# Kernel optimization log

Hardware: AMD Instinct MI355X
Metric: run time of the kernel (lower is better)

Reference implementation:

```python
import jax, jax.numpy as jnp
import numpy as np

N, E, H, L, IN_DIM, OUT_DIM = 50000, 500000, 128, 6, 3, 9


def _lin_init(k, fi, fo):
    W = jax.random.normal(k, (fi, fo), jnp.float32) / np.sqrt(fi)
    return W, jnp.zeros((fo,), jnp.float32)


def setup_inputs() -> dict:
    key = jax.random.key(0)
    ks = jax.random.split(key, 40)
    inp = {}
    inp['x'] = jax.random.normal(ks[0], (N, IN_DIM), jnp.float32)
    inp['coords'] = jax.random.uniform(ks[1], (N, 3), jnp.float32)
    inp['edge_index'] = jax.random.randint(ks[2], (2, E), 0, N, jnp.int64)
    # encoders
    inp['W_ne1'], inp['b_ne1'] = _lin_init(ks[3], IN_DIM, H)
    inp['W_ne2'], inp['b_ne2'] = _lin_init(ks[4], H, H)
    inp['W_ee1'], inp['b_ee1'] = _lin_init(ks[5], 4, H)
    inp['W_ee2'], inp['b_ee2'] = _lin_init(ks[6], H, H)
    # per-layer params, stacked over L
    def stack(fn):
        Ws, bs = zip(*[fn(l) for l in range(L)])
        return jnp.stack(Ws), jnp.stack(bs)
    inp['We1'], inp['be1'] = stack(lambda l: _lin_init(ks[7 + l], 3 * H, H))
    inp['We2'], inp['be2'] = stack(lambda l: _lin_init(ks[13 + l], H, H))
    inp['Wn1'], inp['bn1'] = stack(lambda l: _lin_init(ks[19 + l], 2 * H, H))
    inp['Wn2'], inp['bn2'] = stack(lambda l: _lin_init(ks[25 + l], H, H))
    inp['ln_g'] = jnp.ones((L, H), jnp.float32)
    inp['ln_b'] = jnp.zeros((L, H), jnp.float32)
    # decoder
    inp['Wd1'], inp['bd1'] = _lin_init(ks[31], H, H)
    inp['Wd2'], inp['bd2'] = _lin_init(ks[32], H, OUT_DIM)
    return inp


def _mlp2(x, W1, b1, W2, b2):
    return jax.nn.silu(x @ W1 + b1) @ W2 + b2


def _layernorm(x, g, b, eps=1e-5):
    m = jnp.mean(x, -1, keepdims=True)
    v = jnp.mean(jnp.square(x - m), -1, keepdims=True)
    return (x - m) / jnp.sqrt(v + eps) * g + b


def reference(x, coords, edge_index,
              W_ne1, b_ne1, W_ne2, b_ne2, W_ee1, b_ee1, W_ee2, b_ee2,
              We1, be1, We2, be2, Wn1, bn1, Wn2, bn2, ln_g, ln_b,
              Wd1, bd1, Wd2, bd2):
    src, dst = edge_index[0], edge_index[1]
    # edge features: relative displacement + distance -> (E,4)
    rel = coords[dst] - coords[src]
    ef = jnp.concatenate([rel, jnp.linalg.norm(rel, axis=-1, keepdims=True)], -1)
    edge_attr = _mlp2(ef, W_ee1, b_ee1, W_ee2, b_ee2)  # (E,H)
    h = _mlp2(x, W_ne1, b_ne1, W_ne2, b_ne2)           # (N,H)
    # in-degree for mean aggregation (PyG mean -> 0 for isolated nodes)
    deg = jax.ops.segment_sum(jnp.ones((E,), h.dtype), dst, num_segments=N)
    denom = jnp.maximum(deg, 1.0)[:, None]
    for l in range(L):
        # message: phi_e(x_i=h[dst], x_j=h[src], e_ij)
        m_in = jnp.concatenate([h[dst], h[src], edge_attr], -1)  # (E,3H)
        msg = _mlp2(m_in, We1[l], be1[l], We2[l], be2[l])        # (E,H)
        agg = jax.ops.segment_sum(msg, dst, num_segments=N) / denom
        upd = _mlp2(jnp.concatenate([h, agg], -1), Wn1[l], bn1[l], Wn2[l], bn2[l])
        h = _layernorm(upd + h, ln_g[l], ln_b[l])
    return _mlp2(h, Wd1, bd1, Wd2, bd2)  # (N,out_dim)
```

## Files before the change

### kernel.cpp

```cpp
#include <hip/hip_runtime.h>

#define NN 50000
#define NE 500000
#define HD 128

typedef _Float16 f16;
typedef _Float16 f16x8 __attribute__((ext_vector_type(8)));
typedef _Float16 f16x4 __attribute__((ext_vector_type(4)));
typedef float f32x4 __attribute__((ext_vector_type(4)));


__device__ __forceinline__ int swz(int r, int c) {
  return r * HD + ((((c >> 3) ^ r) & 15) << 3) + (c & 7);
}

__device__ __forceinline__ float fast_silu(float x) {
  return x * __builtin_amdgcn_rcpf(1.0f + __expf(-x));
}

__device__ __forceinline__ void gemm_wave_g(const f16* A, const f16* __restrict__ Wg,
                                            int wstride, int rowBase, int colBase,
                                            f32x4 acc[2][4]) {
  const int lane = (int)threadIdx.x & 63;
  const int m = lane & 15;
  const int q = lane >> 4;
#pragma unroll
  for (int kc = 0; kc < 4; ++kc) {
    const int pc = (((kc * 4 + q) ^ m) & 15) << 3;
    const int gk = (kc * 4 + q) << 3;
    f16x8 a0 = *(const f16x8*)(A + (rowBase + m) * HD + pc);
    f16x8 a1 = *(const f16x8*)(A + (rowBase + 16 + m) * HD + pc);
#pragma unroll
    for (int ct = 0; ct < 4; ++ct) {
      f16x8 b = *(const f16x8*)(Wg + (colBase + ct * 16 + m) * wstride + gk);
      acc[0][ct] = __builtin_amdgcn_mfma_f32_16x16x32_f16(a0, b, acc[0][ct], 0, 0, 0);
      acc[1][ct] = __builtin_amdgcn_mfma_f32_16x16x32_f16(a1, b, acc[1][ct], 0, 0, 0);
    }
  }
}

__device__ __forceinline__ void gemm_wave_g2(const f16* A, const f16* __restrict__ Wg,
                                             int wstride, int rowBase, int colBase,
                                             f32x4 acc[2][2]) {
  const int lane = (int)threadIdx.x & 63;
  const int m = lane & 15;
  const int q = lane >> 4;
#pragma unroll
  for (int kc = 0; kc < 4; ++kc) {
    const int pc = (((kc * 4 + q) ^ m) & 15) << 3;
    const int gk = (kc * 4 + q) << 3;
    f16x8 a0 = *(const f16x8*)(A + (rowBase + m) * HD + pc);
    f16x8 a1 = *(const f16x8*)(A + (rowBase + 16 + m) * HD + pc);
#pragma unroll
    for (int ct = 0; ct < 2; ++ct) {
      f16x8 b = *(const f16x8*)(Wg + (colBase + ct * 16 + m) * wstride + gk);
      acc[0][ct] = __builtin_amdgcn_mfma_f32_16x16x32_f16(a0, b, acc[0][ct], 0, 0, 0);
      acc[1][ct] = __builtin_amdgcn_mfma_f32_16x16x32_f16(a1, b, acc[1][ct], 0, 0, 0);
    }
  }
}

#define ZACC(acc)                                        \
  {                                                      \
    _Pragma("unroll") for (int zi = 0; zi < 2; ++zi)     \
        _Pragma("unroll") for (int zj = 0; zj < 4; ++zj) \
            acc[zi][zj] = (f32x4){0.f, 0.f, 0.f, 0.f};   \
  }

#define ZACC2(acc)                                       \
  {                                                      \
    _Pragma("unroll") for (int zi = 0; zi < 2; ++zi)     \
        _Pragma("unroll") for (int zj = 0; zj < 2; ++zj) \
            acc[zi][zj] = (f32x4){0.f, 0.f, 0.f, 0.f};   \
  }

template <int TPB>
__device__ __forceinline__ void stage_rows64(const f16* __restrict__ g, long r0,
                                             long lim, f16* lds) {
#pragma unroll
  for (int it = 0; it < 1024 / TPB; ++it) {
    int idx = it * TPB + (int)threadIdx.x;
    int r = idx >> 4, ck = idx & 15;
    f16x8 v = {};
    if (r0 + r < lim) v = *(const f16x8*)(g + (r0 + r) * HD + ck * 8);
    *(f16x8*)(lds + r * HD + (((ck ^ r) & 15) << 3)) = v;
  }
}
template <int TPB>
__device__ __forceinline__ void store_rows64(const f16* lds, f16* __restrict__ g,
                                             long r0, long lim) {
#pragma unroll
  for (int it = 0; it < 1024 / TPB; ++it) {
    int idx = it * TPB + (int)threadIdx.x;
    int r = idx >> 4, ck = idx & 15;
    if (r0 + r < lim)
      *(f16x8*)(g + (r0 + r) * HD + ck * 8) =
          *(const f16x8*)(lds + r * HD + (((ck ^ r) & 15) << 3));
  }
}

struct TJob {
  const float* src;
  f16* dst;
  int idim;
  int odim;
};
struct TJobs {
  TJob j[27];
};

__global__ __launch_bounds__(256) void k_prep(TJobs jobs) {
  int job = blockIdx.x >> 2;
  int part = blockIdx.x & 3;
  TJob J = jobs.j[job];
  int total = J.idim * J.odim;
  for (int idx = part * 256 + (int)threadIdx.x; idx < total; idx += 1024) {
    int o = idx / J.idim;
    int i = idx - o * J.idim;
    J.dst[idx] = (f16)J.src[(long)i * J.odim + o];
  }
}

__global__ __launch_bounds__(128) void k_prep_M(const float* __restrict__ Wee2,
                                                const float* __restrict__ b2,
                                                const float* __restrict__ We1,
                                                f16* __restrict__ Mt,
                                                float* __restrict__ cv) {
  __shared__ float col[128];
  int l = blockIdx.x >> 7, o = blockIdx.x & 127;
  int t = threadIdx.x;
  col[t] = We1[((size_t)l * 384 + 256 + t) * 128 + o];
  __syncthreads();
  float s = 0.f;
#pragma unroll 8
  for (int e = 0; e < 128; ++e) s += Wee2[t * 128 + e] * col[e];
  Mt[((size_t)l * 128 + o) * 128 + t] = (f16)s;
  if (t == 0) {
    float c = 0.f;
    for (int e = 0; e < 128; ++e) c += b2[e] * col[e];
    cv[l * 128 + o] = c;
  }
}

__global__ __launch_bounds__(128) void k_prep_Z(const float* __restrict__ We2,
                                                const float* __restrict__ be2,
                                                const float* __restrict__ Wn1,
                                                f16* __restrict__ WZt,
                                                float* __restrict__ bve) {
  __shared__ float col[128];
  int l = blockIdx.x >> 7, o = blockIdx.x & 127;
  int t = threadIdx.x;
  col[t] = Wn1[((size_t)l * 256 + 128 + t) * 128 + o];
  __syncthreads();
  float s = 0.f;
#pragma unroll 8
  for (int j = 0; j < 128; ++j) s += We2[(size_t)l * 128 * 128 + t * 128 + j] * col[j];
  WZt[((size_t)l * 128 + o) * 128 + t] = (f16)s;
  if (t == 0) {
    float c = 0.f;
    for (int j = 0; j < 128; ++j) c += be2[l * 128 + j] * col[j];
    bve[l * 128 + o] = c;
  }
}

__global__ __launch_bounds__(256) void k_hist(const int* __restrict__ dst,
                                              int* __restrict__ count) {
  int e = blockIdx.x * 256 + threadIdx.x;
  if (e < NE) atomicAdd(&count[dst[e]], 1);
}

__global__ __launch_bounds__(1024) void k_scan(const int* __restrict__ count,
                                               int* __restrict__ startA) {
  __shared__ int lds[1024];
  const int CH = 49;
  int t = threadIdx.x;
  int b = t * CH;
  int e = b + CH < NN ? b + CH : NN;
  int s = 0;
  for (int i = b; i < e; ++i) s += count[i];
  lds[t] = s;
  __syncthreads();
  for (int off = 1; off < 1024; off <<= 1) {
    int v = (t >= off) ? lds[t - off] : 0;
    __syncthreads();
    lds[t] += v;
    __syncthreads();
  }
  int run = lds[t] - s;
  for (int i = b; i < e; ++i) {
    startA[i] = run;
    run += count[i];
  }
  if (t == 0) startA[NN] = NE;
}

__global__ __launch_bounds__(256) void k_scatter(const int* __restrict__ src,
                                                 const int* __restrict__ dst,
                                                 const float* __restrict__ coords,
                                                 const int* __restrict__ startA,
                                                 int* __restrict__ cursor,
                                                 int* __restrict__ srcS,
                                                 int* __restrict__ dstS,
                                                 float* __restrict__ efS) {
  int e = blockIdx.x * 256 + threadIdx.x;
  if (e >= NE) return;
  int s = src[e];
  int n = dst[e];
  int pos = startA[n] + atomicAdd(&cursor[n], 1);
  srcS[pos] = s;
  dstS[pos] = n;
  float rx = coords[n * 3] - coords[s * 3];
  float ry = coords[n * 3 + 1] - coords[s * 3 + 1];
  float rz = coords[n * 3 + 2] - coords[s * 3 + 2];
  float nr = sqrtf(rx * rx + ry * ry + rz * rz);
  float4 v;
  v.x = rx;
  v.y = ry;
  v.z = rz;
  v.w = nr;
  *(float4*)(efS + (long)pos * 4) = v;
}

__global__ __launch_bounds__(256, 4) void k_enc_node(
    const float* __restrict__ x, const float* __restrict__ W1,
    const float* __restrict__ b1, const f16* __restrict__ W2t,
    const float* __restrict__ b2, float* __restrict__ h32, f16* __restrict__ h16) {
  __shared__ __align__(16) f16 lds_A[64 * HD];
  __shared__ __align__(16) f16 lds_O[64 * HD];
  float* lds_x = (float*)lds_O;
  long r0 = (long)blockIdx.x * 64;
  int t = threadIdx.x;
  int wv = t >> 6, lane = t & 63, nn = lane & 15, q = lane >> 4;
  int rowBase = (wv >> 1) * 32, colBase = (wv & 1) * 64;

  if (t < 192) {
    long i = r0 * 3 + t;
    lds_x[t] = (i < (long)NN * 3) ? x[i] : 0.f;
  }
  __syncthreads();

  for (int it = 0; it < 32; ++it) {
    int idx = it * 256 + t;
    int r = idx >> 7, c = idx & 127;
    float a = b1[c];
    a += lds_x[r * 3 + 0] * W1[0 * HD + c];
    a += lds_x[r * 3 + 1] * W1[1 * HD + c];
    a += lds_x[r * 3 + 2] * W1[2 * HD + c];
    lds_A[swz(r, c)] = (f16)fast_silu(a);
  }
  __syncthreads();

  f32x4 acc[2][4];
  ZACC(acc);
  gemm_wave_g(lds_A, W2t, HD, rowBase, colBase, acc);
#pragma unroll
  for (int rt = 0; rt < 2; ++rt)
#pragma unroll
    for (int ct = 0; ct < 4; ++ct)
#pragma unroll
      for (int rg = 0; rg < 4; ++rg) {
        int row = rowBase + rt * 16 + q * 4 + rg;
        int col = colBase + ct * 16 + nn;
        float v = acc[rt][ct][rg] + b2[col];
        long nr = r0 + row;
        if (nr < NN) h32[nr * HD + col] = v;
        lds_O[swz(row, col)] = (f16)v;
      }
  __syncthreads();
  store_rows64<256>(lds_O, h16, r0, NN);
}

__global__ __launch_bounds__(512, 8) void k_pp(const f16* __restrict__ h16,
                                               const f16* __restrict__ We1t,
                                               const float* __restrict__ be1,
                                               f16* __restrict__ Pd,
                                               f16* __restrict__ Ps) {
  __shared__ __align__(16) f16 lds_A[64 * HD];
  __shared__ __align__(16) f16 lds_O[64 * HD];
  long r0 = (long)blockIdx.x * 64;
  int t = threadIdx.x;
  int wv = t >> 6, lane = t & 63, nn = lane & 15, q = lane >> 4;
  int rowBase = (wv >> 2) * 32, colBase = (wv & 3) * 32;

  stage_rows64<512>(h16, r0, NN, lds_A);
  __syncthreads();

  f32x4 acc[2][2];
  ZACC2(acc);
  gemm_wave_g2(lds_A, We1t, 384, rowBase, colBase, acc);
#pragma unroll
  for (int rt = 0; rt < 2; ++rt)
#pragma unroll
    for (int ct = 0; ct < 2; ++ct)
#pragma unroll
      for (int rg = 0; rg < 4; ++rg) {
        int row = rowBase + rt * 16 + q * 4 + rg;
        int col = colBase + ct * 16 + nn;
        lds_O[swz(row, col)] = (f16)(acc[rt][ct][rg] + be1[col]);
      }
  __syncthreads();
  store_rows64<512>(lds_O, Pd, r0, NN);

  ZACC2(acc);
  gemm_wave_g2(lds_A, We1t + 128, 384, rowBase, colBase, acc);
  __syncthreads();
#pragma unroll
  for (int rt = 0; rt < 2; ++rt)
#pragma unroll
    for (int ct = 0; ct < 2; ++ct)
#pragma unroll
      for (int rg = 0; rg < 4; ++rg) {
        int row = rowBase + rt * 16 + q * 4 + rg;
        int col = colBase + ct * 16 + nn;
        lds_O[swz(row, col)] = (f16)acc[rt][ct][rg];
      }
  __syncthreads();
  store_rows64<512>(lds_O, Ps, r0, NN);
}

__global__ __launch_bounds__(512, 8) void k_edge(
    const float* __restrict__ efS, const int* __restrict__ srcS,
    const int* __restrict__ dstS, const f16* __restrict__ Pd,
    const f16* __restrict__ Ps, const float* __restrict__ W1,
    const float* __restrict__ b1, const f16* __restrict__ Mt,
    const float* __restrict__ cvec, float* __restrict__ zs) {
  __shared__ __align__(16) f16 lds_A[64 * HD];
  __shared__ __align__(16) f16 lds_P[64 * HD];
  __shared__ __align__(16) float efl[64 * 4];
  __shared__ int dstL[64];
  long e0 = (long)blockIdx.x * 64;
  int t = threadIdx.x;
  int lane = t & 63, nn = lane & 15, q = lane >> 4;
  int wv = t >> 6;
  int rowBase = (wv >> 2) * 32, colBase = (wv & 3) * 32;

  int cc = t & 127;
  float w0 = W1[0 * HD + cc], w1 = W1[1 * HD + cc];
  float w2 = W1[2 * HD + cc], w3 = W1[3 * HD + cc];
  float bb = b1[cc];

  if (t < 64) {
    long e = e0 + t;
    float4 v = {};
    int dd = -1;
    if (e < NE) {
      v = *(const float4*)(efS + e * 4);
      dd = dstS[e];
    }
    *(float4*)(efl + t * 4) = v;
    dstL[t] = dd;
  }

  int rr0 = t >> 4, rr1 = 32 + (t >> 4);
  int ck = t & 15;
  f16x8 pa0 = {}, pb0 = {}, pa1 = {}, pb1 = {};
  {
    long e = e0 + rr0;
    if (e < NE) {
      int d = dstS[e], s = srcS[e];
      pa0 = *(const f16x8*)(Pd + (long)d * HD + ck * 8);
      pb0 = *(const f16x8*)(Ps + (long)s * HD + ck * 8);
    }
  }
  {
    long e = e0 + rr1;
    if (e < NE) {
      int d = dstS[e], s = srcS[e];
      pa1 = *(const f16x8*)(Pd + (long)d * HD + ck * 8);
      pb1 = *(const f16x8*)(Ps + (long)s * HD + ck * 8);
    }
  }
  __syncthreads();

#pragma unroll 4
  for (int it = 0; it < 16; ++it) {
    int r = it * 4 + (t >> 7);
    float a = bb;
    a += efl[r * 4 + 0] * w0;
    a += efl[r * 4 + 1] * w1;
    a += efl[r * 4 + 2] * w2;
    a += efl[r * 4 + 3] * w3;
    lds_A[swz(r, cc)] = (f16)fast_silu(a);
  }
  {
    f16x8 v = pa0 + pb0;
    *(f16x8*)(lds_P + rr0 * HD + (((ck ^ rr0) & 15) << 3)) = v;
  }
  {
    f16x8 v = pa1 + pb1;
    *(f16x8*)(lds_P + rr1 * HD + (((ck ^ rr1) & 15) << 3)) = v;
  }
  __syncthreads();

  f32x4 acc[2][2];
  ZACC2(acc);
  gemm_wave_g2(lds_A, Mt, HD, rowBase, colBase, acc);

#pragma unroll
  for (int rt = 0; rt < 2; ++rt)
#pragma unroll
    for (int ct = 0; ct < 2; ++ct)
#pragma unroll
      for (int rg = 0; rg < 4; ++rg) {
        int row = rowBase + rt * 16 + q * 4 + rg;
        int col = colBase + ct * 16 + nn;
        float v = acc[rt][ct][rg] + (float)lds_P[swz(row, col)] + cvec[col];
        lds_P[swz(row, col)] = (f16)fast_silu(v);
      }
  __syncthreads();

  {
    int c = t & 127, qt = t >> 7;
    int rb = qt * 16;
    int prev = dstL[rb];
    float sum = 0.f;
    for (int r = rb; r < rb + 16; ++r) {
      int d = dstL[r];
      if (d != prev) {
        if (prev >= 0) atomicAdd(&zs[(long)prev * HD + c], sum);
        sum = 0.f;
        prev = d;
      }
      sum += (float)lds_P[swz(r, c)];
    }
    if (prev >= 0) atomicAdd(&zs[(long)prev * HD + c], sum);
  }
}

__global__ __launch_bounds__(256, 4) void k_node(
    const f16* __restrict__ h16in, float* __restrict__ zsum,
    const int* __restrict__ startA, const f16* __restrict__ Wn1t,
    const float* __restrict__ bn1, const f16* __restrict__ WZt,
    const float* __restrict__ bve, const f16* __restrict__ Wn2t,
    const float* __restrict__ bn2, const float* __restrict__ lg,
    const float* __restrict__ lb, float* __restrict__ h32,
    f16* __restrict__ h16out) {
  __shared__ __align__(16) f16 lds_A[64 * HD];
  __shared__ __align__(16) f16 lds_B[64 * HD];
  __shared__ float lds_s[512];
  __shared__ float degf[64];
  long r0 = (long)blockIdx.x * 64;
  int t = threadIdx.x;
  int wv = t >> 6, lane = t & 63, nn = lane & 15, q = lane >> 4;
  int rowBase = (wv >> 1) * 32, colBase = (wv & 1) * 64;

  stage_rows64<256>(h16in, r0, NN, lds_A);
#pragma unroll
  for (int it = 0; it < 8; ++it) {
    int idx = it * 256 + t;
    int r = idx >> 5, c4 = (idx & 31) * 4;
    long nr = r0 + r;
    f16x4 v = {};
    if (nr < NN) {
      float deg = (float)(startA[nr + 1] - startA[nr]);
      float inv = __builtin_amdgcn_rcpf(fmaxf(deg, 1.0f));
      float4 a = *(const float4*)(zsum + nr * HD + c4);
      *(float4*)(zsum + nr * HD + c4) = (float4){0.f, 0.f, 0.f, 0.f};
      v[0] = (f16)(a.x * inv);
      v[1] = (f16)(a.y * inv);
      v[2] = (f16)(a.z * inv);
      v[3] = (f16)(a.w * inv);
      if (c4 == 0) degf[r] = deg > 0.f ? 1.f : 0.f;
    } else if (c4 == 0) {
      degf[r] = 0.f;
    }
    *(f16x4*)(lds_B + swz(r, c4)) = v;
  }
  __syncthreads();

  f32x4 acc[2][4];
  ZACC(acc);
  gemm_wave_g(lds_A, Wn1t, 256, rowBase, colBase, acc);
  gemm_wave_g(lds_B, WZt, HD, rowBase, colBase, acc);
  __syncthreads();

#pragma unroll
  for (int rt = 0; rt < 2; ++rt)
#pragma unroll
    for (int ct = 0; ct < 4; ++ct)
#pragma unroll
      for (int rg = 0; rg < 4; ++rg) {
        int row = rowBase + rt * 16 + q * 4 + rg;
        int col = colBase + ct * 16 + nn;
        lds_B[swz(row, col)] =
            (f16)fast_silu(acc[rt][ct][rg] + bn1[col] + degf[row] * bve[col]);
      }
  __syncthreads();

  ZACC(acc);
  gemm_wave_g(lds_B, Wn2t, HD, rowBase, colBase, acc);

  float vv[2][4][4];
  float s1[8], s2[8];
#pragma unroll
  for (int i = 0; i < 8; ++i) {
    s1[i] = 0.f;
    s2[i] = 0.f;
  }
#pragma unroll
  for (int rt = 0; rt < 2; ++rt)
#pragma unroll
    for (int ct = 0; ct < 4; ++ct)
#pragma unroll
      for (int rg = 0; rg < 4; ++rg) {
        int row = rowBase + rt * 16 + q * 4 + rg;
        int col = colBase + ct * 16 + nn;
        long nr = r0 + row;
        float hv = (nr < NN) ? h32[nr * HD + col] : 0.f;
        float v = acc[rt][ct][rg] + bn2[col] + hv;
        vv[rt][ct][rg] = v;
        s1[rt * 4 + rg] += v;
        s2[rt * 4 + rg] += v * v;
      }
#pragma unroll
  for (int msk = 1; msk <= 8; msk <<= 1) {
#pragma unroll
    for (int i = 0; i < 8; ++i) {
      s1[i] += __shfl_xor(s1[i], msk, 64);
      s2[i] += __shfl_xor(s2[i], msk, 64);
    }
  }
  int ch = wv & 1;
  if (nn == 0) {
#pragma unroll
    for (int rt = 0; rt < 2; ++rt)
#pragma unroll
      for (int rg = 0; rg < 4; ++rg) {
        int row = rowBase + rt * 16 + q * 4 + rg;
        lds_s[row * 2 + ch] = s1[rt * 4 + rg];
        lds_s[256 + row * 2 + ch] = s2[rt * 4 + rg];
      }
  }
  __syncthreads();
#pragma unroll
  for (int rt = 0; rt < 2; ++rt)
#pragma unroll
    for (int ct = 0; ct < 4; ++ct)
#pragma unroll
      for (int rg = 0; rg < 4; ++rg) {
        int row = rowBase + rt * 16 + q * 4 + rg;
        int col = colBase + ct * 16 + nn;
        long nr = r0 + row;
        float S1 = lds_s[row * 2] + lds_s[row * 2 + 1];
        float S2 = lds_s[256 + row * 2] + lds_s[256 + row * 2 + 1];
        float mean = S1 * (1.0f / 128.0f);
        float var = S2 * (1.0f / 128.0f) - mean * mean;
        float rstd = rsqrtf(var + 1e-5f);
        float y = (vv[rt][ct][rg] - mean) * rstd * lg[col] + lb[col];
        if (nr < NN) h32[nr * HD + col] = y;
        lds_A[swz(row, col)] = (f16)y;
      }
  __syncthreads();
  store_rows64<256>(lds_A, h16out, r0, NN);
}

__global__ __launch_bounds__(256, 4) void k_dec(
    const f16* __restrict__ h16, const f16* __restrict__ Wd1t,
    const float* __restrict__ bd1, const float* __restrict__ Wd2,
    const float* __restrict__ bd2, float* __restrict__ out) {
  __shared__ __align__(16) f16 lds_A[64 * HD];
  __shared__ __align__(16) f16 lds_O[64 * HD];
  long r0 = (long)blockIdx.x * 64;
  int t = threadIdx.x;
  int wv = t >> 6, lane = t & 63, nn = lane & 15, q = lane >> 4;
  int rowBase = (wv >> 1) * 32, colBase = (wv & 1) * 64;

  stage_rows64<256>(h16, r0, NN, lds_A);
  __syncthreads();

  f32x4 acc[2][4];
  ZACC(acc);
  gemm_wave_g(lds_A, Wd1t, HD, rowBase, colBase, acc);
#pragma unroll
  for (int rt = 0; rt < 2; ++rt)
#pragma unroll
    for (int ct = 0; ct < 4; ++ct)
#pragma unroll
      for (int rg = 0; rg < 4; ++rg) {
        int row = rowBase + rt * 16 + q * 4 + rg;
        int col = colBase + ct * 16 + nn;
        lds_O[swz(row, col)] = (f16)fast_silu(acc[rt][ct][rg] + bd1[col]);
      }
  __syncthreads();

  for (int idx = t; idx < 64 * 9; idx += 256) {
    int r = idx / 9;
    int o = idx - r * 9;
    long nr = r0 + r;
    if (nr < NN) {
      float a = bd2[o];
      for (int k = 0; k < 128; ++k) a += (float)lds_O[swz(r, k)] * Wd2[k * 9 + o];
      out[nr * 9 + o] = a;
    }
  }
}

extern "C" void kernel_launch(void* const* d_in, const int* in_sizes, int n_in,
                              void* d_out, int out_size, void* d_ws, size_t ws_size,
                              hipStream_t stream) {
  (void)in_sizes;
  (void)n_in;
  (void)out_size;
  (void)ws_size;
  const float* x = (const float*)d_in[0];
  const float* coords = (const float*)d_in[1];
  const int* ei = (const int*)d_in[2];
  const float* W_ne1 = (const float*)d_in[3];
  const float* b_ne1 = (const float*)d_in[4];
  const float* W_ne2 = (const float*)d_in[5];
  const float* b_ne2 = (const float*)d_in[6];
  const float* W_ee1 = (const float*)d_in[7];
  const float* b_ee1 = (const float*)d_in[8];
  const float* W_ee2 = (const float*)d_in[9];
  const float* b_ee2 = (const float*)d_in[10];
  const float* We1 = (const float*)d_in[11];
  const float* be1 = (const float*)d_in[12];
  const float* We2 = (const float*)d_in[13];
  const float* be2 = (const float*)d_in[14];
  const float* Wn1 = (const float*)d_in[15];
  const float* bn1 = (const float*)d_in[16];
  const float* Wn2 = (const float*)d_in[17];
  const float* bn2 = (const float*)d_in[18];
  const float* ln_g = (const float*)d_in[19];
  const float* ln_b = (const float*)d_in[20];
  const float* Wd1 = (const float*)d_in[21];
  const float* bd1 = (const float*)d_in[22];
  const float* Wd2 = (const float*)d_in[23];
  const float* bd2 = (const float*)d_in[24];
  float* out = (float*)d_out;

  char* ws = (char*)d_ws;
  size_t off = 0;
  auto alloc = [&](size_t bytes) -> void* {
    void* p = ws + off;
    off = (off + bytes + 255) & ~(size_t)255;
    return p;
  };
  float* h32 = (float*)alloc((size_t)NN * HD * 4);
  f16* h16 = (f16*)alloc((size_t)NN * HD * 2);
  f16* Pd = (f16*)alloc((size_t)NN * HD * 2);
  f16* Ps = (f16*)alloc((size_t)NN * HD * 2);
  float* agg = (float*)alloc((size_t)NN * HD * 4);
  float* efS = (float*)alloc((size_t)NE * 4 * 4);
  int* srcS = (int*)alloc((size_t)NE * 4);
  int* dstS = (int*)alloc((size_t)NE * 4);
  int* count = (int*)alloc((size_t)2 * NN * 4);
  int* cursor = count + NN;
  int* startA = (int*)alloc((size_t)(NN + 1) * 4);
  f16* wt_ne2 = (f16*)alloc(128 * 128 * 2);
  f16* we1t = (f16*)alloc((size_t)6 * 128 * 384 * 2);
  f16* wn1t = (f16*)alloc((size_t)6 * 128 * 256 * 2);
  f16* wn2t = (f16*)alloc((size_t)6 * 128 * 128 * 2);
  f16* wd1t = (f16*)alloc(128 * 128 * 2);
  f16* mt = (f16*)alloc((size_t)6 * 128 * 128 * 2);
  float* cvec = (float*)alloc((size_t)6 * 128 * 4);
  f16* wzt = (f16*)alloc((size_t)6 * 128 * 128 * 2);
  float* bvv = (float*)alloc((size_t)6 * 128 * 4);

  TJobs jobs;
  int nj = 0;
  jobs.j[nj++] = {W_ne2, wt_ne2, 128, 128};
  for (int l = 0; l < 6; ++l)
    jobs.j[nj++] = {We1 + (size_t)l * 384 * 128, we1t + (size_t)l * 128 * 384, 384, 128};
  for (int l = 0; l < 6; ++l)
    jobs.j[nj++] = {Wn1 + (size_t)l * 256 * 128, wn1t + (size_t)l * 128 * 256, 256, 128};
  for (int l = 0; l < 6; ++l)
    jobs.j[nj++] = {Wn2 + (size_t)l * 128 * 128, wn2t + (size_t)l * 128 * 128, 128, 128};
  jobs.j[nj++] = {Wd1, wd1t, 128, 128};

  const int* srcI = ei;
  const int* dstI = ei + NE;
  const int EB = (NE + 255) / 256;
  const int NT = (NN + 63) / 64;
  const int ET = (NE + 63) / 64;

  k_prep<<<nj * 4, 256, 0, stream>>>(jobs);
  k_prep_M<<<6 * 128, 128, 0, stream>>>(W_ee2, b_ee2, We1, mt, cvec);
  k_prep_Z<<<6 * 128, 128, 0, stream>>>(We2, be2, Wn1, wzt, bvv);
  hipMemsetAsync(count, 0, (size_t)2 * NN * 4, stream);
  hipMemsetAsync(agg, 0, (size_t)NN * HD * 4, stream);
  k_hist<<<EB, 256, 0, stream>>>(dstI, count);
  k_scan<<<1, 1024, 0, stream>>>(count, startA);
  k_scatter<<<EB, 256, 0, stream>>>(srcI, dstI, coords, startA, cursor, srcS, dstS, efS);
  k_enc_node<<<NT, 256, 0, stream>>>(x, W_ne1, b_ne1, wt_ne2, b_ne2, h32, h16);

  for (int l = 0; l < 6; ++l) {
    k_pp<<<NT, 512, 0, stream>>>(h16, we1t + (size_t)l * 128 * 384, be1 + l * 128, Pd, Ps);
    k_edge<<<ET, 512, 0, stream>>>(efS, srcS, dstS, Pd, Ps, W_ee1, b_ee1,
                                   mt + (size_t)l * 128 * 128, cvec + l * 128, agg);
    k_node<<<NT, 256, 0, stream>>>(h16, agg, startA, wn1t + (size_t)l * 128 * 256,
                                   bn1 + l * 128, wzt + (size_t)l * 128 * 128,
                                   bvv + l * 128, wn2t + (size_t)l * 128 * 128,
                                   bn2 + l * 128, ln_g + l * 128, ln_b + l * 128, h32, h16);
  }
  k_dec<<<NT, 256, 0, stream>>>(h16, wd1t, bd1, Wd2, bd2, out);
}
```

Measured before the change: 1.396 ms.

## Compute edge encoder layer with MFMA, remap edge blocks per XCD, reduce atomics

The edge encoder's first layer (4→128) now runs as small MFMAs, with edge features stored as padded fp16x8 and weights pre-packed to fp16, instead of a scalar per-row loop through LDS. Edge workgroups are remapped so consecutive edge tiles land on the same XCD, which should improve L2 locality on the sorted destination segments. Interior destination segments inside a 16-row chunk are written with plain stores instead of atomics, and the cvec bias is folded into Pd in k_pp. The fp16 edge features lose precision. The plain stores assume no other block writes those nodes and that agg is zeroed, which holds only for the first layer unless it is re-zeroed elsewhere.

```diff
diff --git a/kernel.cpp b/kernel.cpp
--- a/kernel.cpp
+++ b/kernel.cpp
@@ -121,6 +121,13 @@
   }
 }
 
+__global__ __launch_bounds__(128) void k_prep_E(const float* __restrict__ W,
+                                                f16* __restrict__ W8) {
+  int t = threadIdx.x;
+#pragma unroll
+  for (int i = 0; i < 8; ++i) W8[t * 8 + i] = (i < 4) ? (f16)W[i * 128 + t] : (f16)0.f;
+}
+
 __global__ __launch_bounds__(128) void k_prep_M(const float* __restrict__ Wee2,
                                                 const float* __restrict__ b2,
                                                 const float* __restrict__ We1,
@@ -201,7 +208,7 @@
                                                  int* __restrict__ cursor,
                                                  int* __restrict__ srcS,
                                                  int* __restrict__ dstS,
-                                                 float* __restrict__ efS) {
+                                                 f16* __restrict__ efS) {
   int e = blockIdx.x * 256 + threadIdx.x;
   if (e >= NE) return;
   int s = src[e];
@@ -213,12 +220,12 @@
   float ry = coords[n * 3 + 1] - coords[s * 3 + 1];
   float rz = coords[n * 3 + 2] - coords[s * 3 + 2];
   float nr = sqrtf(rx * rx + ry * ry + rz * rz);
-  float4 v;
-  v.x = rx;
-  v.y = ry;
-  v.z = rz;
-  v.w = nr;
-  *(float4*)(efS + (long)pos * 4) = v;
+  f16x8 v = {};
+  v[0] = (f16)rx;
+  v[1] = (f16)ry;
+  v[2] = (f16)rz;
+  v[3] = (f16)nr;
+  *(f16x8*)(efS + (long)pos * 8) = v;
 }
 
 __global__ __launch_bounds__(256, 4) void k_enc_node(
@@ -273,6 +280,7 @@
 __global__ __launch_bounds__(512, 8) void k_pp(const f16* __restrict__ h16,
                                                const f16* __restrict__ We1t,
                                                const float* __restrict__ be1,
+                                               const float* __restrict__ cvec,
                                                f16* __restrict__ Pd,
                                                f16* __restrict__ Ps) {
   __shared__ __align__(16) f16 lds_A[64 * HD];
@@ -296,7 +304,7 @@
       for (int rg = 0; rg < 4; ++rg) {
         int row = rowBase + rt * 16 + q * 4 + rg;
         int col = colBase + ct * 16 + nn;
-        lds_O[swz(row, col)] = (f16)(acc[rt][ct][rg] + be1[col]);
+        lds_O[swz(row, col)] = (f16)(acc[rt][ct][rg] + be1[col] + cvec[col]);
       }
   __syncthreads();
   store_rows64<512>(lds_O, Pd, r0, NN);
@@ -319,37 +327,44 @@
 }
 
 __global__ __launch_bounds__(512, 8) void k_edge(
-    const float* __restrict__ efS, const int* __restrict__ srcS,
+    const f16* __restrict__ efS, const int* __restrict__ srcS,
     const int* __restrict__ dstS, const f16* __restrict__ Pd,
-    const f16* __restrict__ Ps, const float* __restrict__ W1,
+    const f16* __restrict__ Ps, const f16* __restrict__ W1e8,
     const float* __restrict__ b1, const f16* __restrict__ Mt,
-    const float* __restrict__ cvec, float* __restrict__ zs) {
+    float* __restrict__ zs, int nwg) {
   __shared__ __align__(16) f16 lds_A[64 * HD];
   __shared__ __align__(16) f16 lds_P[64 * HD];
-  __shared__ __align__(16) float efl[64 * 4];
   __shared__ int dstL[64];
-  long e0 = (long)blockIdx.x * 64;
+  int orig = blockIdx.x;
+  int xcd = orig & 7, loc = orig >> 3;
+  int qq = nwg >> 3, rr = nwg & 7;
+  int wg = (xcd < rr ? xcd * (qq + 1) : rr * (qq + 1) + (xcd - rr) * qq) + loc;
+  long e0 = (long)wg * 64;
   int t = threadIdx.x;
   int lane = t & 63, nn = lane & 15, q = lane >> 4;
   int wv = t >> 6;
   int rowBase = (wv >> 2) * 32, colBase = (wv & 3) * 32;
 
-  int cc = t & 127;
-  float w0 = W1[0 * HD + cc], w1 = W1[1 * HD + cc];
-  float w2 = W1[2 * HD + cc], w3 = W1[3 * HD + cc];
-  float bb = b1[cc];
-
   if (t < 64) {
     long e = e0 + t;
-    float4 v = {};
-    int dd = -1;
-    if (e < NE) {
-      v = *(const float4*)(efS + e * 4);
-      dd = dstS[e];
-    }
-    *(float4*)(efl + t * 4) = v;
-    dstL[t] = dd;
-  }
+    dstL[t] = (e < NE) ? dstS[e] : -1;
+  }
+
+  f16x8 ea0 = {}, ea1 = {}, eb0 = {}, eb1 = {};
+  if (q == 0) {
+    long er0 = e0 + rowBase + nn;
+    long er1 = er0 + 16;
+    if (er0 < NE) ea0 = *(const f16x8*)(efS + er0 * 8);
+    if (er1 < NE) ea1 = *(const f16x8*)(efS + er1 * 8);
+    eb0 = *(const f16x8*)(W1e8 + (colBase + nn) * 8);
+    eb1 = *(const f16x8*)(W1e8 + (colBase + 16 + nn) * 8);
+  }
+  f32x4 sacc[2][2];
+  ZACC2(sacc);
+  sacc[0][0] = __builtin_amdgcn_mfma_f32_16x16x32_f16(ea0, eb0, sacc[0][0], 0, 0, 0);
+  sacc[1][0] = __builtin_amdgcn_mfma_f32_16x16x32_f16(ea1, eb0, sacc[1][0], 0, 0, 0);
+  sacc[0][1] = __builtin_amdgcn_mfma_f32_16x16x32_f16(ea0, eb1, sacc[0][1], 0, 0, 0);
+  sacc[1][1] = __builtin_amdgcn_mfma_f32_16x16x32_f16(ea1, eb1, sacc[1][1], 0, 0, 0);
 
   int rr0 = t >> 4, rr1 = 32 + (t >> 4);
   int ck = t & 15;
@@ -370,17 +385,21 @@
       pb1 = *(const f16x8*)(Ps + (long)s * HD + ck * 8);
     }
   }
-  __syncthreads();
-
-#pragma unroll 4
-  for (int it = 0; it < 16; ++it) {
-    int r = it * 4 + (t >> 7);
-    float a = bb;
-    a += efl[r * 4 + 0] * w0;
-    a += efl[r * 4 + 1] * w1;
-    a += efl[r * 4 + 2] * w2;
-    a += efl[r * 4 + 3] * w3;
-    lds_A[swz(r, cc)] = (f16)fast_silu(a);
+
+  {
+    float b1v0 = b1[colBase + nn], b1v1 = b1[colBase + 16 + nn];
+#pragma unroll
+    for (int rt = 0; rt < 2; ++rt)
+#pragma unroll
+      for (int ct = 0; ct < 2; ++ct) {
+        float bb = ct ? b1v1 : b1v0;
+        int col = colBase + ct * 16 + nn;
+#pragma unroll
+        for (int rg = 0; rg < 4; ++rg) {
+          int row = rowBase + rt * 16 + q * 4 + rg;
+          lds_A[swz(row, col)] = (f16)fast_silu(sacc[rt][ct][rg] + bb);
+        }
+      }
   }
   {
     f16x8 v = pa0 + pb0;
@@ -404,7 +423,7 @@
       for (int rg = 0; rg < 4; ++rg) {
         int row = rowBase + rt * 16 + q * 4 + rg;
         int col = colBase + ct * 16 + nn;
-        float v = acc[rt][ct][rg] + (float)lds_P[swz(row, col)] + cvec[col];
+        float v = acc[rt][ct][rg] + (float)lds_P[swz(row, col)];
         lds_P[swz(row, col)] = (f16)fast_silu(v);
       }
   __syncthreads();
@@ -412,12 +431,18 @@
   {
     int c = t & 127, qt = t >> 7;
     int rb = qt * 16;
-    int prev = dstL[rb];
+    int dfirst = dstL[rb], dlast = dstL[rb + 15];
+    int prev = dfirst;
     float sum = 0.f;
     for (int r = rb; r < rb + 16; ++r) {
       int d = dstL[r];
       if (d != prev) {
-        if (prev >= 0) atomicAdd(&zs[(long)prev * HD + c], sum);
+        if (prev >= 0) {
+          if (prev == dfirst || prev == dlast)
+            atomicAdd(&zs[(long)prev * HD + c], sum);
+          else
+            zs[(long)prev * HD + c] = sum;
+        }
         sum = 0.f;
         prev = d;
       }
@@ -641,7 +666,7 @@
   f16* Pd = (f16*)alloc((size_t)NN * HD * 2);
   f16* Ps = (f16*)alloc((size_t)NN * HD * 2);
   float* agg = (float*)alloc((size_t)NN * HD * 4);
-  float* efS = (float*)alloc((size_t)NE * 4 * 4);
+  f16* efS = (f16*)alloc((size_t)NE * 8 * 2);
   int* srcS = (int*)alloc((size_t)NE * 4);
   int* dstS = (int*)alloc((size_t)NE * 4);
   int* count = (int*)alloc((size_t)2 * NN * 4);
@@ -656,6 +681,7 @@
   float* cvec = (float*)alloc((size_t)6 * 128 * 4);
   f16* wzt = (f16*)alloc((size_t)6 * 128 * 128 * 2);
   float* bvv = (float*)alloc((size_t)6 * 128 * 4);
+  f16* w1e8 = (f16*)alloc(128 * 8 * 2);
 
   TJobs jobs;
   int nj = 0;
@@ -675,6 +701,7 @@
   const int ET = (NE + 63) / 64;
 
   k_prep<<<nj * 4, 256, 0, stream>>>(jobs);
+  k_prep_E<<<1, 128, 0, stream>>>(W_ee1, w1e8);
   k_prep_M<<<6 * 128, 128, 0, stream>>>(W_ee2, b_ee2, We1, mt, cvec);
   k_prep_Z<<<6 * 128, 128, 0, stream>>>(We2, be2, Wn1, wzt, bvv);
   hipMemsetAsync(count, 0, (size_t)2 * NN * 4, stream);
@@ -685,9 +712,10 @@
   k_enc_node<<<NT, 256, 0, stream>>>(x, W_ne1, b_ne1, wt_ne2, b_ne2, h32, h16);
 
   for (int l = 0; l < 6; ++l) {
-    k_pp<<<NT, 512, 0, stream>>>(h16, we1t + (size_t)l * 128 * 384, be1 + l * 128, Pd, Ps);
-    k_edge<<<ET, 512, 0, stream>>>(efS, srcS, dstS, Pd, Ps, W_ee1, b_ee1,
-                                   mt + (size_t)l * 128 * 128, cvec + l * 128, agg);
+    k_pp<<<NT, 512, 0, stream>>>(h16, we1t + (size_t)l * 128 * 384, be1 + l * 128,
+                                 cvec + l * 128, Pd, Ps);
+    k_edge<<<ET, 512, 0, stream>>>(efS, srcS, dstS, Pd, Ps, w1e8, b_ee1,
+                                   mt + (size_t)l * 128 * 128, agg, ET);
     k_node<<<NT, 256, 0, stream>>>(h16, agg, startA, wn1t + (size_t)l * 128 * 256,
                                    bn1 + l * 128, wzt + (size_t)l * 128 * 128,
                                    bvv + l * 128, wn2t + (size_t)l * 128 * 128,
```

Measured after the change: 1.323 ms. 5.3% less time.
